# Kernel optimization log

Measured on AMD Instinct MI355X. Metric: run time of the kernel, lower is better.

Reference implementation:

```python
import jax, jax.numpy as jnp
import numpy as np

B, S, E, D = 256, 256, 2, 128  # batch, seq_len, encoder_dim, decoder_dim


def setup_inputs() -> dict:
    key = jax.random.key(0)
    ks = jax.random.split(key, 9)
    u = lambda k, shape, n: jax.random.uniform(k, shape, jnp.float32, -1.0 / np.sqrt(n), 1.0 / np.sqrt(n))
    return {
        "out_encoder": jax.random.normal(ks[0], (B, S, E), jnp.float32),
        "W1_w": u(ks[1], (S, S), S),            # Linear(seq_len, seq_len)
        "W1_b": u(ks[2], (S,), S),
        "W2_w": u(ks[3], (S, 2 * S), 2 * S),    # Linear(2*seq_len, seq_len)
        "W2_b": u(ks[4], (S,), 2 * S),
        "W_ih": u(ks[5], (4 * D, E), D),        # LSTMCell input weights (i,f,g,o)
        "W_hh": u(ks[6], (4 * D, D), D),
        "b_ih": u(ks[7], (4 * D,), D),
        "b_hh": u(ks[8], (4 * D,), D),
    }


def reference(out_encoder, W1_w, W1_b, W2_w, W2_b, W_ih, W_hh, b_ih, b_hh):
    b, s, e = out_encoder.shape
    d = W_hh.shape[1]
    dt = out_encoder.dtype

    # W_2 term: encoder flattened to [B, 2S]; identical every step, hoist it.
    w2term = out_encoder.reshape(b, s * e) @ W2_w.T + W2_b          # [B, S]
    # W_1 applied to a row of S copies of h_d equals h_d * rowsum(W1) + b.
    w1sum = W1_w.sum(axis=1)                                        # [S]

    def attn(h):  # h: [B, D] -> context [B, E]
        hterm = h[:, :, None] * w1sum[None, None, :] + W1_b         # [B, D, S]
        en = jnp.tanh(w2term[:, None, :] + hterm)                   # [B, D, S]
        alpha = jax.nn.softmax(en, axis=-1).mean(axis=1)            # [B, S] (softmax over seq)
        return jnp.einsum('bs,bse->be', alpha, out_encoder)         # [B, E]

    def lstm_cell(x, h, c):
        gates = x @ W_ih.T + h @ W_hh.T + b_ih + b_hh               # [B, 4D]
        i, f, g, o = jnp.split(gates, 4, axis=-1)
        c = jax.nn.sigmoid(f) * c + jax.nn.sigmoid(i) * jnp.tanh(g)
        h = jax.nn.sigmoid(o) * jnp.tanh(c)
        return h, c

    h0 = jnp.zeros((b, d), dt)
    c0 = jnp.zeros((b, d), dt)

    def step(carry, _):
        h, c = carry
        x = attn(h)
        h, c = lstm_cell(x, h, c)
        return (h, c), h

    _, hs = jax.lax.scan(step, (h0, c0), None, length=s)
    return hs  # [S, B, D]: stacked decoder hidden states (original returns a list of h_t)
```

## Files before the change

kernel.cpp:

```cpp
#include <hip/hip_runtime.h>

#define NB 256
#define NS 256
#define NE 2
#define ND 128
#define NT 512
#define NN 16
#define SLOTH 160

typedef float vf4 __attribute__((ext_vector_type(4)));
typedef _Float16 f16x8 __attribute__((ext_vector_type(8)));
typedef float f32x4 __attribute__((ext_vector_type(4)));

constexpr float L2E = 1.4426950408889634f;
constexpr float PI_F = 3.14159265358979323846f;

__device__ const float CT[16][16] = {
 {1,0,0,0,0,0,0,0,0,0,0,0,0,0,0,0},
 {0,1,0,0,0,0,0,0,0,0,0,0,0,0,0,0},
 {-1,0,2,0,0,0,0,0,0,0,0,0,0,0,0,0},
 {0,-3,0,4,0,0,0,0,0,0,0,0,0,0,0,0},
 {1,0,-8,0,8,0,0,0,0,0,0,0,0,0,0,0},
 {0,5,0,-20,0,16,0,0,0,0,0,0,0,0,0,0},
 {-1,0,18,0,-48,0,32,0,0,0,0,0,0,0,0,0},
 {0,-7,0,56,0,-112,0,64,0,0,0,0,0,0,0,0},
 {1,0,-32,0,160,0,-256,0,128,0,0,0,0,0,0,0},
 {0,9,0,-120,0,432,0,-576,0,256,0,0,0,0,0},
 {-1,0,50,0,-400,0,1120,0,-1280,0,512,0,0,0,0,0},
 {0,-11,0,220,0,-1232,0,2816,0,-2816,0,1024,0,0,0,0},
 {1,0,-72,0,840,0,-3584,0,6912,0,-6144,0,2048,0,0,0},
 {0,13,0,-364,0,2912,0,-9984,0,16640,0,-13312,0,4096,0,0},
 {-1,0,98,0,-1568,0,9408,0,-26880,0,39424,0,-28672,0,8192,0},
 {0,-15,0,560,0,-6048,0,28800,0,-70400,0,92160,0,-61440,0,16384}};

template <int C>
__device__ __forceinline__ float dppadd(float x) {
    return x + __builtin_bit_cast(float,
        __builtin_amdgcn_update_dpp(0, __builtin_bit_cast(int, x), C, 0xF, 0xF, true));
}
__device__ __forceinline__ float red_oct(float x) {
    x = dppadd<0xB1>(x); x = dppadd<0x4E>(x); x = dppadd<0x141>(x); return x;
}
__device__ __forceinline__ float red_wave64(float x) {
    x = dppadd<0xB1>(x); x = dppadd<0x4E>(x); x = dppadd<0x141>(x);
    x = dppadd<0x140>(x); x = dppadd<0x142>(x); x = dppadd<0x143>(x); return x;
}
__device__ __forceinline__ float red_half32(float x) {
    x = dppadd<0xB1>(x); x = dppadd<0x4E>(x); x = dppadd<0x141>(x);
    x = dppadd<0x140>(x); x = dppadd<0x142>(x); return x;
}

__global__ __launch_bounds__(NT, 2)
void attn_lstm_decoder(const float* __restrict__ enc,
                       const float* __restrict__ W1w,
                       const float* __restrict__ W1b,
                       const float* __restrict__ W2w,
                       const float* __restrict__ W2b,
                       const float* __restrict__ Wih,
                       const float* __restrict__ Whh,
                       const float* __restrict__ bih,
                       const float* __restrict__ bhh,
                       float* __restrict__ out)
{
    const int b    = blockIdx.x;
    const int t    = threadIdx.x;
    const int wave = t >> 6;
    const int lane = t & 63;
    const int grp  = lane >> 4;
    const int nib  = lane & 15;
    const int gl   = 16 * wave + nib;
    const bool qb0 = grp & 1;
    const bool qb1 = grp & 2;
    const int half = lane >> 5;
    const int idx  = lane & 31;
    const int jnode = 2 * wave + half;

    __shared__ __align__(16) _Float16 hist16[2 * SLOTH];
    __shared__ __align__(16) float xwbuf[2][16];
    __shared__ float A2_l[NS];
    __shared__ float g2_l[NS];
    __shared__ float e0_l[NS];
    __shared__ float e1_l[NS];
    __shared__ float Ml[NN * NN];
    __shared__ float2 Pn[NN];
    __shared__ float2 Vl[NN];
    __shared__ float Pm0[NN], Pm1[NN];

    {
        float v = enc[b * (NS * NE) + t];
        if (t & 1) e1_l[t >> 1] = v; else e0_l[t >> 1] = v;
    }
    if (t < NN * NN) {
        const int mi = t >> 4, mj = t & 15;
        const float w = (mi == 0) ? (1.0f / NN) : (2.0f / NN);
        Ml[t] = w * __cosf((float)(mi * (2 * mj + 1)) * (PI_F / (2 * NN)));
    }
    __syncthreads();

    for (int r = 0; r < 32; ++r) {
        const int s = wave * 32 + r;
        float p = W1w[s * NS + lane]       + W1w[s * NS + lane + 64]
                + W1w[s * NS + lane + 128] + W1w[s * NS + lane + 192];
        p = red_wave64(p);
        if (lane == 63) g2_l[s] = p * (2.0f * L2E);
        float qq = 0.0f;
        #pragma unroll
        for (int kk = 0; kk < 8; ++kk) {
            const int c = lane + kk * 64;
            const float ev = (c & 1) ? e1_l[c >> 1] : e0_l[c >> 1];
            qq = fmaf(ev, W2w[s * (2 * NS) + c], qq);
        }
        qq = red_wave64(qq);
        if (lane == 63) A2_l[s] = (qq + W2b[s] + W1b[s]) * (2.0f * L2E);
    }
    __syncthreads();

    {
        const float y  = __cosf((float)(2 * jnode + 1) * (PI_F / (2 * NN)));
        const float C2 = -2.0f * L2E;
        float l = 0.0f, p0 = 0.0f, p1 = 0.0f;
        #pragma unroll
        for (int k = 0; k < 8; ++k) {
            const int s = k * 32 + idx;
            const float m1 = fmaf(y, g2_l[s], A2_l[s]);
            const float u  = __builtin_amdgcn_exp2f(m1);
            const float rc = __builtin_amdgcn_rcpf(u + 1.0f);
            const float e  = __builtin_amdgcn_exp2f(rc * C2);
            l += e;
            p0 = fmaf(e, e0_l[s], p0);
            p1 = fmaf(e, e1_l[s], p1);
        }
        l = red_half32(l); p0 = red_half32(p0); p1 = red_half32(p1);
        if ((lane & 31) == 31) {
            const float rl = __builtin_amdgcn_rcpf(l);
            Pn[jnode] = make_float2(p0 * rl, p1 * rl);
        }
    }
    __syncthreads();

    if (t < NN) {
        float v0 = 0.0f, v1 = 0.0f;
        #pragma unroll
        for (int j = 0; j < NN; ++j) {
            v0 = fmaf(Ml[t * NN + j], Pn[j].x, v0);
            v1 = fmaf(Ml[t * NN + j], Pn[j].y, v1);
        }
        Vl[t] = make_float2(v0 * (1.0f / ND), v1 * (1.0f / ND));
    }

    f16x8 wf[4][4];
    #pragma unroll
    for (int rt = 0; rt < 4; ++rt) {
        const int row = 128 * rt + 16 * wave + nib;
        #pragma unroll
        for (int kt = 0; kt < 4; ++kt) {
            const vf4 wa = *reinterpret_cast<const vf4*>(Whh + row * ND + 32 * kt + 8 * grp);
            const vf4 wb = *reinterpret_cast<const vf4*>(Whh + row * ND + 32 * kt + 8 * grp + 4);
            f16x8 wv;
            wv[0] = (_Float16)wa.x; wv[1] = (_Float16)wa.y;
            wv[2] = (_Float16)wa.z; wv[3] = (_Float16)wa.w;
            wv[4] = (_Float16)wb.x; wv[5] = (_Float16)wb.y;
            wv[6] = (_Float16)wb.z; wv[7] = (_Float16)wb.w;
            wf[rt][kt] = wv;
        }
    }
    float wi0_[4], wi1_[4], bb_[4];
    #pragma unroll
    for (int j = 0; j < 4; ++j) {
        const int r = 128 * j + gl;
        wi0_[j] = Wih[r * 2 + 0];
        wi1_[j] = Wih[r * 2 + 1];
        bb_[j]  = bih[r] + bhh[r];
    }

    if (t < ND) hist16[SLOTH + 40 * (t >> 5) + (t & 31)] = (_Float16)0.0f;
    float h_reg = 0.0f, c_reg = 0.0f;
    __syncthreads();

    if (t < NN) {
        float s0 = 0.0f, s1 = 0.0f;
        #pragma unroll
        for (int k = 0; k < NN; ++k) {
            s0 = fmaf(Vl[k].x, CT[k][t], s0);
            s1 = fmaf(Vl[k].y, CT[k][t], s1);
        }
        Pm0[t] = s0; Pm1[t] = s1;
    }
    __syncthreads();

    float Q0[4], Q1[4];
    #pragma unroll
    for (int i = 0; i < 4; ++i) { Q0[i] = Pm0[4 * i + grp]; Q1[i] = Pm1[4 * i + grp]; }

    auto phaseG = [&](float h, int pw) {
        const float h2 = h * h;
        const float h3 = h2 * h;
        const float h4 = h2 * h2;
        const float hq = qb1 ? (qb0 ? h3 : h2) : (qb0 ? h : 1.0f);
        float a0 = fmaf(Q0[3], h4, Q0[2]);
        a0 = fmaf(a0, h4, Q0[1]);
        a0 = fmaf(a0, h4, Q0[0]);
        float a1 = fmaf(Q1[3], h4, Q1[2]);
        a1 = fmaf(a1, h4, Q1[1]);
        a1 = fmaf(a1, h4, Q1[0]);
        a0 *= hq;
        a1 *= hq;
        a0 = red_wave64(a0); a1 = red_wave64(a1);
        if (lane == 63) {
            xwbuf[pw][2 * wave + 0] = a0;
            xwbuf[pw][2 * wave + 1] = a1;
        }
    };

    phaseG(0.0f, 0);
    __syncthreads();

    const int hoff = 40 * (gl >> 5) + (gl & 31);

    for (int step = 0; step < NS; ++step) {
        const int pr = step & 1;
        const int rs = pr ^ 1;
        const int ws = pr;

        f16x8 af[4];
        const _Float16* hsl = &hist16[rs * SLOTH + 8 * grp];
        #pragma unroll
        for (int kt = 0; kt < 4; ++kt)
            af[kt] = __builtin_bit_cast(f16x8,
                *reinterpret_cast<const int4*>(hsl + 40 * kt));

        float2 xv = *reinterpret_cast<const float2*>(&xwbuf[pr][2 * (lane & 7)]);
        const float x0 = red_oct(xv.x);
        const float x1 = red_oct(xv.y);
        float bt[4];
        #pragma unroll
        for (int j = 0; j < 4; ++j)
            bt[j] = fmaf(x0, wi0_[j], fmaf(x1, wi1_[j], bb_[j]));

        float ga[4];
        #pragma unroll
        for (int rt = 0; rt < 4; ++rt) {
            f32x4 a0 = {0.0f, 0.0f, 0.0f, 0.0f};
            f32x4 a1 = {0.0f, 0.0f, 0.0f, 0.0f};
            a0 = __builtin_amdgcn_mfma_f32_16x16x32_f16(af[0], wf[rt][0], a0, 0, 0, 0);
            a1 = __builtin_amdgcn_mfma_f32_16x16x32_f16(af[2], wf[rt][2], a1, 0, 0, 0);
            a0 = __builtin_amdgcn_mfma_f32_16x16x32_f16(af[1], wf[rt][1], a0, 0, 0, 0);
            a1 = __builtin_amdgcn_mfma_f32_16x16x32_f16(af[3], wf[rt][3], a1, 0, 0, 0);
            ga[rt] = a0[0] + a1[0];
        }

        const float gi = ga[0] + bt[0];
        const float gf = ga[1] + bt[1];
        const float gg = ga[2] + bt[2];
        const float go = ga[3] + bt[3];

        const float si = __builtin_amdgcn_rcpf(1.0f + __builtin_amdgcn_exp2f(-L2E * gi));
        const float sf = __builtin_amdgcn_rcpf(1.0f + __builtin_amdgcn_exp2f(-L2E * gf));
        const float so = __builtin_amdgcn_rcpf(1.0f + __builtin_amdgcn_exp2f(-L2E * go));
        const float tg = 1.0f - 2.0f * __builtin_amdgcn_rcpf(
            __builtin_amdgcn_exp2f(2.0f * L2E * gg) + 1.0f);
        c_reg = fmaf(sf, c_reg, si * tg);
        const float tc2 = 1.0f - 2.0f * __builtin_amdgcn_rcpf(
            __builtin_amdgcn_exp2f(2.0f * L2E * c_reg) + 1.0f);
        h_reg = so * tc2;

        if (grp == 0) {
            hist16[ws * SLOTH + hoff] = (_Float16)h_reg;
            out[(size_t)step * (NB * ND) + b * ND + gl] = h_reg;
        }
        phaseG(h_reg, pr ^ 1);

        asm volatile("s_waitcnt lgkmcnt(0)" ::: "memory");
        __builtin_amdgcn_s_barrier();
    }
}

extern "C" void kernel_launch(void* const* d_in, const int* in_sizes, int n_in,
                              void* d_out, int out_size, void* d_ws, size_t ws_size,
                              hipStream_t stream) {
    const float* enc = (const float*)d_in[0];
    const float* W1w = (const float*)d_in[1];
    const float* W1b = (const float*)d_in[2];
    const float* W2w = (const float*)d_in[3];
    const float* W2b = (const float*)d_in[4];
    const float* Wih = (const float*)d_in[5];
    const float* Whh = (const float*)d_in[6];
    const float* bih = (const float*)d_in[7];
    const float* bhh = (const float*)d_in[8];
    attn_lstm_decoder<<<NB, NT, 0, stream>>>(enc, W1w, W1b, W2w, W2b,
                                             Wih, Whh, bih, bhh, (float*)d_out);
}
```

Before: 271.0 us.

## Compute attention polynomial redundantly per wave from h history, drop xwbuf exchange

Each wave now reads the full previous hidden state from LDS and evaluates the degree-15 attention polynomial itself, reducing across the wave with DPP and bpermute. This removes the per-wave partial-sum buffer and the cross-wave reduction that previously followed the LSTM update, taking that work off the serial step's critical path. The history buffer loses its padded layout and the MFMA chain uses one accumulator instead of two. In exchange every wave repeats the polynomial work, the plain layout may cause LDS bank conflicts, and the single accumulator chain lengthens the MFMA dependency.

```diff
diff --git a/kernel.cpp b/kernel.cpp
--- a/kernel.cpp
+++ b/kernel.cpp
@@ -6,10 +6,10 @@
 #define ND 128
 #define NT 512
 #define NN 16
-#define SLOTH 160
 
 typedef float vf4 __attribute__((ext_vector_type(4)));
 typedef _Float16 f16x8 __attribute__((ext_vector_type(8)));
+typedef _Float16 f16x2 __attribute__((ext_vector_type(2)));
 typedef float f32x4 __attribute__((ext_vector_type(4)));
 
 constexpr float L2E = 1.4426950408889634f;
@@ -38,9 +38,6 @@
     return x + __builtin_bit_cast(float,
         __builtin_amdgcn_update_dpp(0, __builtin_bit_cast(int, x), C, 0xF, 0xF, true));
 }
-__device__ __forceinline__ float red_oct(float x) {
-    x = dppadd<0xB1>(x); x = dppadd<0x4E>(x); x = dppadd<0x141>(x); return x;
-}
 __device__ __forceinline__ float red_wave64(float x) {
     x = dppadd<0xB1>(x); x = dppadd<0x4E>(x); x = dppadd<0x141>(x);
     x = dppadd<0x140>(x); x = dppadd<0x142>(x); x = dppadd<0x143>(x); return x;
@@ -48,6 +45,13 @@
 __device__ __forceinline__ float red_half32(float x) {
     x = dppadd<0xB1>(x); x = dppadd<0x4E>(x); x = dppadd<0x141>(x);
     x = dppadd<0x140>(x); x = dppadd<0x142>(x); return x;
+}
+__device__ __forceinline__ float red16_all(float x) {
+    x = dppadd<0xB1>(x);
+    x = dppadd<0x4E>(x);
+    x = dppadd<0x141>(x);
+    x = dppadd<0x140>(x);
+    return x;
 }
 
 __global__ __launch_bounds__(NT, 2)
@@ -69,14 +73,11 @@
     const int grp  = lane >> 4;
     const int nib  = lane & 15;
     const int gl   = 16 * wave + nib;
-    const bool qb0 = grp & 1;
-    const bool qb1 = grp & 2;
     const int half = lane >> 5;
     const int idx  = lane & 31;
     const int jnode = 2 * wave + half;
 
-    __shared__ __align__(16) _Float16 hist16[2 * SLOTH];
-    __shared__ __align__(16) float xwbuf[2][16];
+    __shared__ __align__(16) _Float16 hist16[2 * ND];
     __shared__ float A2_l[NS];
     __shared__ float g2_l[NS];
     __shared__ float e0_l[NS];
@@ -173,7 +174,7 @@
         bb_[j]  = bih[r] + bhh[r];
     }
 
-    if (t < ND) hist16[SLOTH + 40 * (t >> 5) + (t & 31)] = (_Float16)0.0f;
+    if (t < ND) hist16[ND + t] = (_Float16)0.0f;
     float h_reg = 0.0f, c_reg = 0.0f;
     __syncthreads();
 
@@ -188,71 +189,62 @@
     }
     __syncthreads();
 
-    float Q0[4], Q1[4];
+    float C0[16], C1[16];
     #pragma unroll
-    for (int i = 0; i < 4; ++i) { Q0[i] = Pm0[4 * i + grp]; Q1[i] = Pm1[4 * i + grp]; }
-
-    auto phaseG = [&](float h, int pw) {
+    for (int i = 0; i < 16; ++i) { C0[i] = Pm0[i]; C1[i] = Pm1[i]; }
+
+    auto evalG = [&](float h, const float (&C)[16]) -> float {
         const float h2 = h * h;
-        const float h3 = h2 * h;
-        const float h4 = h2 * h2;
-        const float hq = qb1 ? (qb0 ? h3 : h2) : (qb0 ? h : 1.0f);
-        float a0 = fmaf(Q0[3], h4, Q0[2]);
-        a0 = fmaf(a0, h4, Q0[1]);
-        a0 = fmaf(a0, h4, Q0[0]);
-        float a1 = fmaf(Q1[3], h4, Q1[2]);
-        a1 = fmaf(a1, h4, Q1[1]);
-        a1 = fmaf(a1, h4, Q1[0]);
-        a0 *= hq;
-        a1 *= hq;
-        a0 = red_wave64(a0); a1 = red_wave64(a1);
-        if (lane == 63) {
-            xwbuf[pw][2 * wave + 0] = a0;
-            xwbuf[pw][2 * wave + 1] = a1;
-        }
+        float e = C[14], o = C[15];
+        #pragma unroll
+        for (int k = 12; k >= 0; k -= 2) {
+            e = fmaf(e, h2, C[k]);
+            o = fmaf(o, h2, C[k + 1]);
+        }
+        return fmaf(h, o, e);
     };
 
-    phaseG(0.0f, 0);
-    __syncthreads();
-
-    const int hoff = 40 * (gl >> 5) + (gl & 31);
+    const int jpair = 32 * (nib >> 2) + 8 * grp + 2 * (nib & 3);
+    const int idx16 = ((lane ^ 16) << 2);
+    const int idx32 = ((lane ^ 32) << 2);
 
     for (int step = 0; step < NS; ++step) {
-        const int pr = step & 1;
-        const int rs = pr ^ 1;
-        const int ws = pr;
-
-        f16x8 af[4];
-        const _Float16* hsl = &hist16[rs * SLOTH + 8 * grp];
-        #pragma unroll
-        for (int kt = 0; kt < 4; ++kt)
-            af[kt] = __builtin_bit_cast(f16x8,
-                *reinterpret_cast<const int4*>(hsl + 40 * kt));
-
-        float2 xv = *reinterpret_cast<const float2*>(&xwbuf[pr][2 * (lane & 7)]);
-        const float x0 = red_oct(xv.x);
-        const float x1 = red_oct(xv.y);
-        float bt[4];
-        #pragma unroll
-        for (int j = 0; j < 4; ++j)
-            bt[j] = fmaf(x0, wi0_[j], fmaf(x1, wi1_[j], bb_[j]));
+        const int rs = (step & 1) ^ 1;
+        const int ws = step & 1;
+        const _Float16* hb = &hist16[rs * ND];
+
+        const f16x8 af0 = __builtin_bit_cast(f16x8, *reinterpret_cast<const int4*>(hb + 0  + 8 * grp));
+        const f16x8 af1 = __builtin_bit_cast(f16x8, *reinterpret_cast<const int4*>(hb + 32 + 8 * grp));
+        const f16x8 af2 = __builtin_bit_cast(f16x8, *reinterpret_cast<const int4*>(hb + 64 + 8 * grp));
+        const f16x8 af3 = __builtin_bit_cast(f16x8, *reinterpret_cast<const int4*>(hb + 96 + 8 * grp));
+        const f16x2 hp2 = *reinterpret_cast<const f16x2*>(hb + jpair);
+
+        const float ha = (float)hp2[0];
+        const float hc = (float)hp2[1];
+        float r0 = evalG(ha, C0) + evalG(hc, C0);
+        float r1 = evalG(ha, C1) + evalG(hc, C1);
+        r0 = red16_all(r0); r1 = red16_all(r1);
+        r0 += __builtin_bit_cast(float, __builtin_amdgcn_ds_bpermute(idx16, __builtin_bit_cast(int, r0)));
+        r1 += __builtin_bit_cast(float, __builtin_amdgcn_ds_bpermute(idx16, __builtin_bit_cast(int, r1)));
+        r0 += __builtin_bit_cast(float, __builtin_amdgcn_ds_bpermute(idx32, __builtin_bit_cast(int, r0)));
+        r1 += __builtin_bit_cast(float, __builtin_amdgcn_ds_bpermute(idx32, __builtin_bit_cast(int, r1)));
+        const float x0 = r0, x1 = r1;
 
         float ga[4];
         #pragma unroll
         for (int rt = 0; rt < 4; ++rt) {
-            f32x4 a0 = {0.0f, 0.0f, 0.0f, 0.0f};
-            f32x4 a1 = {0.0f, 0.0f, 0.0f, 0.0f};
-            a0 = __builtin_amdgcn_mfma_f32_16x16x32_f16(af[0], wf[rt][0], a0, 0, 0, 0);
-            a1 = __builtin_amdgcn_mfma_f32_16x16x32_f16(af[2], wf[rt][2], a1, 0, 0, 0);
-            a0 = __builtin_amdgcn_mfma_f32_16x16x32_f16(af[1], wf[rt][1], a0, 0, 0, 0);
-            a1 = __builtin_amdgcn_mfma_f32_16x16x32_f16(af[3], wf[rt][3], a1, 0, 0, 0);
-            ga[rt] = a0[0] + a1[0];
-        }
-
-        const float gi = ga[0] + bt[0];
-        const float gf = ga[1] + bt[1];
-        const float gg = ga[2] + bt[2];
-        const float go = ga[3] + bt[3];
+            f32x4 a = {0.0f, 0.0f, 0.0f, 0.0f};
+            a = __builtin_amdgcn_mfma_f32_16x16x32_f16(af0, wf[rt][0], a, 0, 0, 0);
+            a = __builtin_amdgcn_mfma_f32_16x16x32_f16(af1, wf[rt][1], a, 0, 0, 0);
+            a = __builtin_amdgcn_mfma_f32_16x16x32_f16(af2, wf[rt][2], a, 0, 0, 0);
+            a = __builtin_amdgcn_mfma_f32_16x16x32_f16(af3, wf[rt][3], a, 0, 0, 0);
+            ga[rt] = a[0];
+        }
+
+        const float gi = ga[0] + fmaf(x0, wi0_[0], fmaf(x1, wi1_[0], bb_[0]));
+        const float gf = ga[1] + fmaf(x0, wi0_[1], fmaf(x1, wi1_[1], bb_[1]));
+        const float gg = ga[2] + fmaf(x0, wi0_[2], fmaf(x1, wi1_[2], bb_[2]));
+        const float go = ga[3] + fmaf(x0, wi0_[3], fmaf(x1, wi1_[3], bb_[3]));
 
         const float si = __builtin_amdgcn_rcpf(1.0f + __builtin_amdgcn_exp2f(-L2E * gi));
         const float sf = __builtin_amdgcn_rcpf(1.0f + __builtin_amdgcn_exp2f(-L2E * gf));
@@ -265,10 +257,9 @@
         h_reg = so * tc2;
 
         if (grp == 0) {
-            hist16[ws * SLOTH + hoff] = (_Float16)h_reg;
+            hist16[ws * ND + gl] = (_Float16)h_reg;
             out[(size_t)step * (NB * ND) + b * ND + gl] = h_reg;
         }
-        phaseG(h_reg, pr ^ 1);
 
         asm volatile("s_waitcnt lgkmcnt(0)" ::: "memory");
         __builtin_amdgcn_s_barrier();
```

New measurement: 312.1 us. +15.2%, slower.

## Halve workgroup to 4 waves, each wave computing 32 hidden units per step

Applied to the files above, without the earlier changes.

The block size drops from 512 to 256 threads. Each wave now issues twice as many MFMAs, covering 32 hidden units with two 16-row tiles, and the Chebyshev attention polynomial is split across two lane copies instead of four. The aim is to cut per-step barrier and cross-wave reduction cost: fewer waves sync, and the x reduction shrinks from 8 to 4 partials. In exchange each wave carries more weight registers and a longer serial MFMA chain per step, and half the lanes compute results that are discarded.

```diff
diff --git a/kernel.cpp b/kernel.cpp
--- a/kernel.cpp
+++ b/kernel.cpp
@@ -4,9 +4,8 @@
 #define NS 256
 #define NE 2
 #define ND 128
-#define NT 512
+#define NT 256
 #define NN 16
-#define SLOTH 160
 
 typedef float vf4 __attribute__((ext_vector_type(4)));
 typedef _Float16 f16x8 __attribute__((ext_vector_type(8)));
@@ -38,19 +37,22 @@
     return x + __builtin_bit_cast(float,
         __builtin_amdgcn_update_dpp(0, __builtin_bit_cast(int, x), C, 0xF, 0xF, true));
 }
-__device__ __forceinline__ float red_oct(float x) {
-    x = dppadd<0xB1>(x); x = dppadd<0x4E>(x); x = dppadd<0x141>(x); return x;
+__device__ __forceinline__ float red_quad(float x) {
+    x = dppadd<0xB1>(x); x = dppadd<0x4E>(x); return x;
 }
 __device__ __forceinline__ float red_wave64(float x) {
     x = dppadd<0xB1>(x); x = dppadd<0x4E>(x); x = dppadd<0x141>(x);
     x = dppadd<0x140>(x); x = dppadd<0x142>(x); x = dppadd<0x143>(x); return x;
 }
-__device__ __forceinline__ float red_half32(float x) {
-    x = dppadd<0xB1>(x); x = dppadd<0x4E>(x); x = dppadd<0x141>(x);
-    x = dppadd<0x140>(x); x = dppadd<0x142>(x); return x;
-}
-
-__global__ __launch_bounds__(NT, 2)
+__device__ __forceinline__ float red16_all(float x) {
+    x = dppadd<0xB1>(x);
+    x = dppadd<0x4E>(x);
+    x = dppadd<0x141>(x);
+    x = dppadd<0x140>(x);
+    return x;
+}
+
+__global__ __launch_bounds__(NT, 1)
 void attn_lstm_decoder(const float* __restrict__ enc,
                        const float* __restrict__ W1w,
                        const float* __restrict__ W1b,
@@ -68,15 +70,12 @@
     const int lane = t & 63;
     const int grp  = lane >> 4;
     const int nib  = lane & 15;
-    const int gl   = 16 * wave + nib;
-    const bool qb0 = grp & 1;
-    const bool qb1 = grp & 2;
-    const int half = lane >> 5;
-    const int idx  = lane & 31;
-    const int jnode = 2 * wave + half;
-
-    __shared__ __align__(16) _Float16 hist16[2 * SLOTH];
-    __shared__ __align__(16) float xwbuf[2][16];
+    const int sub  = grp & 1;
+    const int cpy  = grp >> 1;
+    const int gl   = 32 * wave + 16 * sub + nib;
+
+    __shared__ __align__(16) _Float16 hist16[2 * ND];
+    __shared__ __align__(16) float xwbuf[2][8];
     __shared__ float A2_l[NS];
     __shared__ float g2_l[NS];
     __shared__ float e0_l[NS];
@@ -86,19 +85,20 @@
     __shared__ float2 Vl[NN];
     __shared__ float Pm0[NN], Pm1[NN];
 
+    #pragma unroll
+    for (int i = t; i < NS * NE; i += NT) {
+        float v = enc[b * (NS * NE) + i];
+        if (i & 1) e1_l[i >> 1] = v; else e0_l[i >> 1] = v;
+    }
     {
-        float v = enc[b * (NS * NE) + t];
-        if (t & 1) e1_l[t >> 1] = v; else e0_l[t >> 1] = v;
-    }
-    if (t < NN * NN) {
         const int mi = t >> 4, mj = t & 15;
         const float w = (mi == 0) ? (1.0f / NN) : (2.0f / NN);
         Ml[t] = w * __cosf((float)(mi * (2 * mj + 1)) * (PI_F / (2 * NN)));
     }
     __syncthreads();
 
-    for (int r = 0; r < 32; ++r) {
-        const int s = wave * 32 + r;
+    for (int r = 0; r < 64; ++r) {
+        const int s = wave * 64 + r;
         float p = W1w[s * NS + lane]       + W1w[s * NS + lane + 64]
                 + W1w[s * NS + lane + 128] + W1w[s * NS + lane + 192];
         p = red_wave64(p);
@@ -116,12 +116,13 @@
     __syncthreads();
 
     {
-        const float y  = __cosf((float)(2 * jnode + 1) * (PI_F / (2 * NN)));
+        const int jn = 4 * wave + grp;
+        const float y  = __cosf((float)(2 * jn + 1) * (PI_F / (2 * NN)));
         const float C2 = -2.0f * L2E;
         float l = 0.0f, p0 = 0.0f, p1 = 0.0f;
         #pragma unroll
-        for (int k = 0; k < 8; ++k) {
-            const int s = k * 32 + idx;
+        for (int k = 0; k < 16; ++k) {
+            const int s = k * 16 + nib;
             const float m1 = fmaf(y, g2_l[s], A2_l[s]);
             const float u  = __builtin_amdgcn_exp2f(m1);
             const float rc = __builtin_amdgcn_rcpf(u + 1.0f);
@@ -130,10 +131,10 @@
             p0 = fmaf(e, e0_l[s], p0);
             p1 = fmaf(e, e1_l[s], p1);
         }
-        l = red_half32(l); p0 = red_half32(p0); p1 = red_half32(p1);
-        if ((lane & 31) == 31) {
+        l = red16_all(l); p0 = red16_all(p0); p1 = red16_all(p1);
+        if (nib == 0) {
             const float rl = __builtin_amdgcn_rcpf(l);
-            Pn[jnode] = make_float2(p0 * rl, p1 * rl);
+            Pn[jn] = make_float2(p0 * rl, p1 * rl);
         }
     }
     __syncthreads();
@@ -148,20 +149,23 @@
         Vl[t] = make_float2(v0 * (1.0f / ND), v1 * (1.0f / ND));
     }
 
-    f16x8 wf[4][4];
-    #pragma unroll
-    for (int rt = 0; rt < 4; ++rt) {
-        const int row = 128 * rt + 16 * wave + nib;
-        #pragma unroll
-        for (int kt = 0; kt < 4; ++kt) {
-            const vf4 wa = *reinterpret_cast<const vf4*>(Whh + row * ND + 32 * kt + 8 * grp);
-            const vf4 wb = *reinterpret_cast<const vf4*>(Whh + row * ND + 32 * kt + 8 * grp + 4);
-            f16x8 wv;
-            wv[0] = (_Float16)wa.x; wv[1] = (_Float16)wa.y;
-            wv[2] = (_Float16)wa.z; wv[3] = (_Float16)wa.w;
-            wv[4] = (_Float16)wb.x; wv[5] = (_Float16)wb.y;
-            wv[6] = (_Float16)wb.z; wv[7] = (_Float16)wb.w;
-            wf[rt][kt] = wv;
+    f16x8 wf[4][2][4];
+    #pragma unroll
+    for (int j = 0; j < 4; ++j) {
+        #pragma unroll
+        for (int s = 0; s < 2; ++s) {
+            const int row = 128 * j + 32 * wave + 16 * s + nib;
+            #pragma unroll
+            for (int kt = 0; kt < 4; ++kt) {
+                const vf4 wa = *reinterpret_cast<const vf4*>(Whh + row * ND + 32 * kt + 8 * grp);
+                const vf4 wb = *reinterpret_cast<const vf4*>(Whh + row * ND + 32 * kt + 8 * grp + 4);
+                f16x8 wv;
+                wv[0] = (_Float16)wa.x; wv[1] = (_Float16)wa.y;
+                wv[2] = (_Float16)wa.z; wv[3] = (_Float16)wa.w;
+                wv[4] = (_Float16)wb.x; wv[5] = (_Float16)wb.y;
+                wv[6] = (_Float16)wb.z; wv[7] = (_Float16)wb.w;
+                wf[j][s][kt] = wv;
+            }
         }
     }
     float wi0_[4], wi1_[4], bb_[4];
@@ -173,7 +177,7 @@
         bb_[j]  = bih[r] + bhh[r];
     }
 
-    if (t < ND) hist16[SLOTH + 40 * (t >> 5) + (t & 31)] = (_Float16)0.0f;
+    if (t < 2 * ND) hist16[t] = (_Float16)0.0f;
     float h_reg = 0.0f, c_reg = 0.0f;
     __syncthreads();
 
@@ -188,50 +192,48 @@
     }
     __syncthreads();
 
-    float Q0[4], Q1[4];
-    #pragma unroll
-    for (int i = 0; i < 4; ++i) { Q0[i] = Pm0[4 * i + grp]; Q1[i] = Pm1[4 * i + grp]; }
+    float cc0[8], cc1[8];
+    #pragma unroll
+    for (int i = 0; i < 8; ++i) {
+        cc0[i] = Pm0[2 * i + cpy];
+        cc1[i] = Pm1[2 * i + cpy];
+    }
 
     auto phaseG = [&](float h, int pw) {
         const float h2 = h * h;
-        const float h3 = h2 * h;
-        const float h4 = h2 * h2;
-        const float hq = qb1 ? (qb0 ? h3 : h2) : (qb0 ? h : 1.0f);
-        float a0 = fmaf(Q0[3], h4, Q0[2]);
-        a0 = fmaf(a0, h4, Q0[1]);
-        a0 = fmaf(a0, h4, Q0[0]);
-        float a1 = fmaf(Q1[3], h4, Q1[2]);
-        a1 = fmaf(a1, h4, Q1[1]);
-        a1 = fmaf(a1, h4, Q1[0]);
-        a0 *= hq;
-        a1 *= hq;
-        a0 = red_wave64(a0); a1 = red_wave64(a1);
+        float v0 = cc0[7], v1 = cc1[7];
+        #pragma unroll
+        for (int k = 6; k >= 0; --k) {
+            v0 = fmaf(v0, h2, cc0[k]);
+            v1 = fmaf(v1, h2, cc1[k]);
+        }
+        const float hsel = cpy ? h : 1.0f;
+        v0 *= hsel;
+        v1 *= hsel;
+        v0 = red_wave64(v0); v1 = red_wave64(v1);
         if (lane == 63) {
-            xwbuf[pw][2 * wave + 0] = a0;
-            xwbuf[pw][2 * wave + 1] = a1;
+            xwbuf[pw][2 * wave + 0] = v0;
+            xwbuf[pw][2 * wave + 1] = v1;
         }
     };
 
     phaseG(0.0f, 0);
     __syncthreads();
-
-    const int hoff = 40 * (gl >> 5) + (gl & 31);
 
     for (int step = 0; step < NS; ++step) {
         const int pr = step & 1;
         const int rs = pr ^ 1;
         const int ws = pr;
-
-        f16x8 af[4];
-        const _Float16* hsl = &hist16[rs * SLOTH + 8 * grp];
-        #pragma unroll
-        for (int kt = 0; kt < 4; ++kt)
-            af[kt] = __builtin_bit_cast(f16x8,
-                *reinterpret_cast<const int4*>(hsl + 40 * kt));
-
-        float2 xv = *reinterpret_cast<const float2*>(&xwbuf[pr][2 * (lane & 7)]);
-        const float x0 = red_oct(xv.x);
-        const float x1 = red_oct(xv.y);
+        const _Float16* hb = &hist16[rs * ND];
+
+        const f16x8 af0 = __builtin_bit_cast(f16x8, *reinterpret_cast<const int4*>(hb + 0  + 8 * grp));
+        const f16x8 af1 = __builtin_bit_cast(f16x8, *reinterpret_cast<const int4*>(hb + 32 + 8 * grp));
+        const f16x8 af2 = __builtin_bit_cast(f16x8, *reinterpret_cast<const int4*>(hb + 64 + 8 * grp));
+        const f16x8 af3 = __builtin_bit_cast(f16x8, *reinterpret_cast<const int4*>(hb + 96 + 8 * grp));
+
+        float2 xv = *reinterpret_cast<const float2*>(&xwbuf[pr][2 * (lane & 3)]);
+        const float x0 = red_quad(xv.x);
+        const float x1 = red_quad(xv.y);
         float bt[4];
         #pragma unroll
         for (int j = 0; j < 4; ++j)
@@ -239,14 +241,18 @@
 
         float ga[4];
         #pragma unroll
-        for (int rt = 0; rt < 4; ++rt) {
+        for (int j = 0; j < 4; ++j) {
             f32x4 a0 = {0.0f, 0.0f, 0.0f, 0.0f};
             f32x4 a1 = {0.0f, 0.0f, 0.0f, 0.0f};
-            a0 = __builtin_amdgcn_mfma_f32_16x16x32_f16(af[0], wf[rt][0], a0, 0, 0, 0);
-            a1 = __builtin_amdgcn_mfma_f32_16x16x32_f16(af[2], wf[rt][2], a1, 0, 0, 0);
-            a0 = __builtin_amdgcn_mfma_f32_16x16x32_f16(af[1], wf[rt][1], a0, 0, 0, 0);
-            a1 = __builtin_amdgcn_mfma_f32_16x16x32_f16(af[3], wf[rt][3], a1, 0, 0, 0);
-            ga[rt] = a0[0] + a1[0];
+            a0 = __builtin_amdgcn_mfma_f32_16x16x32_f16(af0, wf[j][0][0], a0, 0, 0, 0);
+            a1 = __builtin_amdgcn_mfma_f32_16x16x32_f16(af0, wf[j][1][0], a1, 0, 0, 0);
+            a0 = __builtin_amdgcn_mfma_f32_16x16x32_f16(af1, wf[j][0][1], a0, 0, 0, 0);
+            a1 = __builtin_amdgcn_mfma_f32_16x16x32_f16(af1, wf[j][1][1], a1, 0, 0, 0);
+            a0 = __builtin_amdgcn_mfma_f32_16x16x32_f16(af2, wf[j][0][2], a0, 0, 0, 0);
+            a1 = __builtin_amdgcn_mfma_f32_16x16x32_f16(af2, wf[j][1][2], a1, 0, 0, 0);
+            a0 = __builtin_amdgcn_mfma_f32_16x16x32_f16(af3, wf[j][0][3], a0, 0, 0, 0);
+            a1 = __builtin_amdgcn_mfma_f32_16x16x32_f16(af3, wf[j][1][3], a1, 0, 0, 0);
+            ga[j] = sub ? a1[0] : a0[0];
         }
 
         const float gi = ga[0] + bt[0];
@@ -264,8 +270,8 @@
             __builtin_amdgcn_exp2f(2.0f * L2E * c_reg) + 1.0f);
         h_reg = so * tc2;
 
-        if (grp == 0) {
-            hist16[ws * SLOTH + hoff] = (_Float16)h_reg;
+        if (cpy == 0) {
+            hist16[ws * ND + gl] = (_Float16)h_reg;
             out[(size_t)step * (NB * ND) + b * ND + gl] = h_reg;
         }
         phaseG(h_reg, pr ^ 1);
```

New measurement: 271.1 us. Within noise of the previous version (+0.0%).
